# Performance work log

Hardware: AMD Instinct MI355X
Metric: run time of the kernel (lower is better)

The kernel has to match this reference:

```python
import jax, jax.numpy as jnp
import numpy as np

NUM_HEADS = 8
HEAD_DIM = 64  # joiner_dim 512 / 8
LN_EPS = 1e-5


def _layer_norm(x, g, b):
    mu = jnp.mean(x, axis=-1, keepdims=True)
    var = jnp.mean(jnp.square(x - mu), axis=-1, keepdims=True)
    return (x - mu) * jax.lax.rsqrt(var + LN_EPS) * g + b


def setup_inputs() -> dict:
    key = jax.random.key(0)
    ks = jax.random.split(key, 24)
    N, T, S = 16, 512, 5
    E, D, J, V = 512, 512, 512, 2000
    s = 0.02
    inp = {
        "encoder_out": jax.random.normal(ks[0], (N, T, S, E), jnp.float32),
        "decoder_out": jax.random.normal(ks[1], (N, T, S, D), jnp.float32),
        # ScaledLinear projections (initial_scale absorbed into weights)
        "We": jax.random.normal(ks[2], (J, E), jnp.float32) * s * 0.25,
        "be": jnp.zeros((J,), jnp.float32),
        "Wd": jax.random.normal(ks[3], (J, D), jnp.float32) * s * 0.25,
        "bd": jnp.zeros((J,), jnp.float32),
        # LayerNorms
        "g_q": jnp.ones((J,), jnp.float32),
        "beta_q": jnp.zeros((J,), jnp.float32),
        "g_kv": jnp.ones((J,), jnp.float32),
        "beta_kv": jnp.zeros((J,), jnp.float32),
        # attention projections (xavier-ish)
        "Wq": jax.random.normal(ks[4], (J, J), jnp.float32) * s,
        "bq": jnp.zeros((J,), jnp.float32),
        "Wk": jax.random.normal(ks[5], (J, J), jnp.float32) * s,
        "bk": jnp.zeros((J,), jnp.float32),
        "Wv": jax.random.normal(ks[6], (J, J), jnp.float32) * s,
        "bv": jnp.zeros((J,), jnp.float32),
        "Wo": jax.random.normal(ks[7], (J, J), jnp.float32) * s,
        "bo": jnp.zeros((J,), jnp.float32),
        # final vocab projection
        "Wout": jax.random.normal(ks[8], (V, J), jnp.float32) * s,
        "bout": jnp.zeros((V,), jnp.float32),
    }
    return inp


def reference(encoder_out, decoder_out, We, be, Wd, bd, g_q, beta_q, g_kv, beta_kv,
              Wq, bq, Wk, bk, Wv, bv, Wo, bo, Wout, bout):
    # input projections (mode == "transducer", project_input=True)
    enc = jnp.einsum('ntsc,jc->ntsj', encoder_out, We) + be
    dec = jnp.einsum('ntsc,jc->ntsj', decoder_out, Wd) + bd

    # framewise sigmoid attention
    q_in = _layer_norm(dec, g_q, beta_q)
    kv_in = _layer_norm(enc, g_kv, beta_kv)
    q = jnp.einsum('ntsj,kj->ntsk', q_in, Wq) + bq
    k = jnp.einsum('ntsj,kj->ntsk', kv_in, Wk) + bk
    v = jnp.einsum('ntsj,kj->ntsk', kv_in, Wv) + bv

    shp = q.shape[:-1]
    q = q.reshape(*shp, NUM_HEADS, HEAD_DIM)
    k = k.reshape(*shp, NUM_HEADS, HEAD_DIM)
    v = v.reshape(*shp, NUM_HEADS, HEAD_DIM)

    scale = HEAD_DIM ** -0.5
    attn = jax.nn.sigmoid(jnp.sum(q * k, axis=-1, keepdims=True) * scale)  # (N,T,S,H,1)
    context = (attn * v).reshape(*shp, NUM_HEADS * HEAD_DIM)
    context = jnp.einsum('ntsj,kj->ntsk', context, Wo) + bo

    h = jnp.tanh(dec + context)
    logits = jnp.einsum('ntsj,vj->ntsv', h, Wout) + bout
    return logits
```

## Files before the change

kernel.cpp:

```cpp
#include <hip/hip_runtime.h>
#include <stdint.h>


typedef __attribute__((ext_vector_type(8))) __bf16 bf16x8;
typedef __attribute__((ext_vector_type(4))) float float4v;
typedef __attribute__((ext_vector_type(8))) unsigned short ushort8;

static constexpr int M_TOT = 16 * 512 * 5;
static constexpr int JDIM  = 512;
static constexpr int VOUT  = 2000;
static constexpr int VPAD  = 2048;

#define DI __device__ __forceinline__

DI float bf2f(unsigned short u) {
    union { unsigned int i; float f; } w; w.i = ((unsigned int)u) << 16; return w.f;
}
DI unsigned short f2bf(float f) {
    union { float f; unsigned int i; } w; w.f = f;
    return (unsigned short)((w.i + 0x8000u) >> 16);
}

DI void gld_lds16(const void* g, void* l) {
    __builtin_amdgcn_global_load_lds(
        reinterpret_cast<__attribute__((address_space(1))) void*>(
            reinterpret_cast<uintptr_t>(g)),
        reinterpret_cast<__attribute__((address_space(3))) void*>(
            reinterpret_cast<uintptr_t>(l)),
        16, 0, 0);
}

template <int EPI, int NOUT, bool A32>
__global__ __launch_bounds__(256) void gemm_bt(
    const void* __restrict__ Ap, const unsigned short* __restrict__ B,
    const float* __restrict__ bias, void* __restrict__ Cp,
    const unsigned short* __restrict__ dres)
{
    constexpr int K = 512;
    constexpr int BM = 128, BN = 128, BK = 32;
    __shared__ unsigned short As[BM * BK];
    __shared__ unsigned short Bs[BN * BK];

    const int tid  = threadIdx.x;
    const int wave = tid >> 6;
    const int lane = tid & 63;
    const int wm   = wave >> 1;
    const int wn   = wave & 1;
    const int quad = lane >> 4;
    const int l16  = lane & 15;

    const int m0 = blockIdx.y * BM;
    const int n0 = blockIdx.x * BN;

    float4v acc[4][4];
#pragma unroll
    for (int i = 0; i < 4; i++)
#pragma unroll
        for (int j = 0; j < 4; j++)
            acc[i][j] = {0.f, 0.f, 0.f, 0.f};

    const float*          Af = (const float*)Ap;
    const unsigned short* Ab = (const unsigned short*)Ap;

    const int c0 = tid, c1 = tid + 256;
    const int ar0 = c0 >> 2, ac0 = (c0 & 3) * 8;
    const int ar1 = c1 >> 2, ac1 = (c1 & 3) * 8;

    for (int k0 = 0; k0 < K; k0 += BK) {
        gld_lds16(&B[(size_t)(n0 + ar0) * K + k0 + ac0], &Bs[c0 * 8]);
        gld_lds16(&B[(size_t)(n0 + ar1) * K + k0 + ac1], &Bs[c1 * 8]);
        if constexpr (A32) {
            const float* p0 = &Af[(size_t)(m0 + ar0) * K + k0 + ac0];
            const float* p1 = &Af[(size_t)(m0 + ar1) * K + k0 + ac1];
            float4 f0 = *(const float4*)p0;
            float4 f1 = *(const float4*)(p0 + 4);
            float4 g0 = *(const float4*)p1;
            float4 g1 = *(const float4*)(p1 + 4);
            ushort8 u0, u1;
            u0[0] = f2bf(f0.x); u0[1] = f2bf(f0.y); u0[2] = f2bf(f0.z); u0[3] = f2bf(f0.w);
            u0[4] = f2bf(f1.x); u0[5] = f2bf(f1.y); u0[6] = f2bf(f1.z); u0[7] = f2bf(f1.w);
            u1[0] = f2bf(g0.x); u1[1] = f2bf(g0.y); u1[2] = f2bf(g0.z); u1[3] = f2bf(g0.w);
            u1[4] = f2bf(g1.x); u1[5] = f2bf(g1.y); u1[6] = f2bf(g1.z); u1[7] = f2bf(g1.w);
            *reinterpret_cast<ushort8*>(&As[c0 * 8]) = u0;
            *reinterpret_cast<ushort8*>(&As[c1 * 8]) = u1;
        } else {
            gld_lds16(&Ab[(size_t)(m0 + ar0) * K + k0 + ac0], &As[c0 * 8]);
            gld_lds16(&Ab[(size_t)(m0 + ar1) * K + k0 + ac1], &As[c1 * 8]);
        }
        __syncthreads();

        bf16x8 af[4], bfv[4];
#pragma unroll
        for (int i = 0; i < 4; i++)
            af[i] = *reinterpret_cast<const bf16x8*>(
                &As[(wm * 64 + i * 16 + l16) * BK + quad * 8]);
#pragma unroll
        for (int j = 0; j < 4; j++)
            bfv[j] = *reinterpret_cast<const bf16x8*>(
                &Bs[(wn * 64 + j * 16 + l16) * BK + quad * 8]);
#pragma unroll
        for (int i = 0; i < 4; i++)
#pragma unroll
            for (int j = 0; j < 4; j++)
                acc[i][j] = __builtin_amdgcn_mfma_f32_16x16x32_bf16(
                    af[i], bfv[j], acc[i][j], 0, 0, 0);
        __syncthreads();
    }

    float bias_v[4];
#pragma unroll
    for (int j = 0; j < 4; j++) {
        int col = n0 + wn * 64 + j * 16 + l16;
        bias_v[j] = (col < NOUT) ? bias[col] : 0.f;
    }

#pragma unroll
    for (int i = 0; i < 4; i++) {
        int rbase = m0 + wm * 64 + i * 16 + quad * 4;
#pragma unroll
        for (int j = 0; j < 4; j++) {
            int col = n0 + wn * 64 + j * 16 + l16;
#pragma unroll
            for (int r = 0; r < 4; r++) {
                float val = acc[i][j][r] + bias_v[j];
                int row = rbase + r;
                if constexpr (EPI == 0) {
                    ((unsigned short*)Cp)[(size_t)row * NOUT + col] = f2bf(val);
                } else if constexpr (EPI == 2) {
                    float d = bf2f(dres[(size_t)row * 512 + col]);
                    ((unsigned short*)Cp)[(size_t)row * 512 + col] = f2bf(tanhf(d + val));
                } else {
                    if (col < NOUT)
                        ((float*)Cp)[(size_t)row * NOUT + col] = val;
                }
            }
        }
    }
}

__global__ __launch_bounds__(256) void wconv_kernel(
    const float* __restrict__ We, const float* __restrict__ Wd,
    const float* __restrict__ Wq, const float* __restrict__ Wk,
    const float* __restrict__ Wv, const float* __restrict__ Wo,
    const float* __restrict__ Wout, unsigned short* __restrict__ WB)
{
#pragma unroll
    for (int t = 0; t < 4; t++) {
        int i = blockIdx.x * 1024 + t * 256 + threadIdx.x;
        float v;
        if (i < 1572864) {
            int seg = i >> 18, off = i & 262143;
            const float* src = seg == 0 ? We : seg == 1 ? Wd : seg == 2 ? Wq
                             : seg == 3 ? Wk : seg == 4 ? Wv : Wo;
            v = src[off];
        } else {
            int rem = i - 1572864;
            int row = rem >> 9;
            v = (row < VOUT) ? Wout[rem] : 0.f;
        }
        WB[i] = f2bf(v);
    }
}

__global__ __launch_bounds__(256) void ln_kernel(
    const unsigned short* __restrict__ decO, const unsigned short* __restrict__ encO,
    const float* __restrict__ g_q, const float* __restrict__ beta_q,
    const float* __restrict__ g_kv, const float* __restrict__ beta_kv,
    unsigned short* __restrict__ q_in, unsigned short* __restrict__ kv_in)
{
    int row  = blockIdx.x * 4 + (threadIdx.x >> 6);
    int lane = threadIdx.x & 63;
    const unsigned short* src; const float *g, *bt; unsigned short* dst; int r;
    if (row < M_TOT) { src = decO; g = g_q;  bt = beta_q;  dst = q_in;  r = row; }
    else             { src = encO; g = g_kv; bt = beta_kv; dst = kv_in; r = row - M_TOT; }

    ushort8 u = *reinterpret_cast<const ushort8*>(&src[(size_t)r * 512 + lane * 8]);
    float x[8]; float s = 0.f, s2 = 0.f;
#pragma unroll
    for (int j = 0; j < 8; j++) { x[j] = bf2f(u[j]); s += x[j]; s2 += x[j] * x[j]; }
#pragma unroll
    for (int m = 1; m < 64; m <<= 1) {
        s  += __shfl_xor(s, m, 64);
        s2 += __shfl_xor(s2, m, 64);
    }
    float mean = s * (1.f / 512.f);
    float var  = s2 * (1.f / 512.f) - mean * mean;
    float rstd = rsqrtf(var + 1e-5f);
    ushort8 o;
#pragma unroll
    for (int j = 0; j < 8; j++) {
        int col = lane * 8 + j;
        o[j] = f2bf((x[j] - mean) * rstd * g[col] + bt[col]);
    }
    *reinterpret_cast<ushort8*>(&dst[(size_t)r * 512 + lane * 8]) = o;
}

__global__ __launch_bounds__(256) void attn_kernel(
    const unsigned short* __restrict__ q, const unsigned short* __restrict__ k,
    const unsigned short* __restrict__ v, unsigned short* __restrict__ ctx)
{
    int row  = blockIdx.x * 4 + (threadIdx.x >> 6);
    int lane = threadIdx.x & 63;
    size_t off = (size_t)row * 512 + lane * 8;
    ushort8 uq = *reinterpret_cast<const ushort8*>(&q[off]);
    ushort8 uk = *reinterpret_cast<const ushort8*>(&k[off]);
    float dot = 0.f;
#pragma unroll
    for (int j = 0; j < 8; j++) dot += bf2f(uq[j]) * bf2f(uk[j]);
    dot += __shfl_xor(dot, 1, 64);
    dot += __shfl_xor(dot, 2, 64);
    dot += __shfl_xor(dot, 4, 64);
    float sg = 1.f / (1.f + __expf(-dot * 0.125f));
    ushort8 uv = *reinterpret_cast<const ushort8*>(&v[off]);
    ushort8 o;
#pragma unroll
    for (int j = 0; j < 8; j++) o[j] = f2bf(sg * bf2f(uv[j]));
    *reinterpret_cast<ushort8*>(&ctx[off]) = o;
}

extern "C" void kernel_launch(void* const* d_in, const int* in_sizes, int n_in,
                              void* d_out, int out_size, void* d_ws, size_t ws_size,
                              hipStream_t stream)
{
    (void)in_sizes; (void)n_in; (void)out_size; (void)ws_size;
    const float* enc_in  = (const float*)d_in[0];
    const float* dec_in  = (const float*)d_in[1];
    const float* We      = (const float*)d_in[2];  const float* be     = (const float*)d_in[3];
    const float* Wd      = (const float*)d_in[4];  const float* bd     = (const float*)d_in[5];
    const float* g_q     = (const float*)d_in[6];  const float* beta_q = (const float*)d_in[7];
    const float* g_kv    = (const float*)d_in[8];  const float* beta_kv= (const float*)d_in[9];
    const float* Wq      = (const float*)d_in[10]; const float* bq     = (const float*)d_in[11];
    const float* Wk      = (const float*)d_in[12]; const float* bk     = (const float*)d_in[13];
    const float* Wv      = (const float*)d_in[14]; const float* bv     = (const float*)d_in[15];
    const float* Wo      = (const float*)d_in[16]; const float* bo     = (const float*)d_in[17];
    const float* Wout    = (const float*)d_in[18]; const float* bout   = (const float*)d_in[19];
    float* out = (float*)d_out;

    unsigned short* WB    = (unsigned short*)d_ws;
    unsigned short* WeB   = WB + 0;
    unsigned short* WdB   = WB + 262144;
    unsigned short* WqB   = WB + 524288;
    unsigned short* WkB   = WB + 786432;
    unsigned short* WvB   = WB + 1048576;
    unsigned short* WoB   = WB + 1310720;
    unsigned short* WoutB = WB + 1572864;

    char* sbase = (char*)d_ws + 5242880;
    const size_t SZ = (size_t)M_TOT * 512 * 2;
    unsigned short* S0 = (unsigned short*)(sbase + 0 * SZ);
    unsigned short* S1 = (unsigned short*)(sbase + 1 * SZ);
    unsigned short* S2 = (unsigned short*)(sbase + 2 * SZ);
    unsigned short* S3 = (unsigned short*)(sbase + 3 * SZ);
    unsigned short* S4 = (unsigned short*)(sbase + 4 * SZ);
    unsigned short* S5 = (unsigned short*)(sbase + 5 * SZ);

    dim3 blk(256);
    dim3 g512(JDIM / 128, M_TOT / 128);
    dim3 gout(VPAD / 128, M_TOT / 128);

    wconv_kernel<<<2560, blk, 0, stream>>>(We, Wd, Wq, Wk, Wv, Wo, Wout, WB);

    gemm_bt<0, 512, true><<<g512, blk, 0, stream>>>(enc_in, WeB, be, S0, nullptr);
    gemm_bt<0, 512, true><<<g512, blk, 0, stream>>>(dec_in, WdB, bd, S1, nullptr);

    ln_kernel<<<(2 * M_TOT) / 4, blk, 0, stream>>>(S1, S0, g_q, beta_q, g_kv, beta_kv, S2, S3);

    gemm_bt<0, 512, false><<<g512, blk, 0, stream>>>(S2, WqB, bq, S4, nullptr);
    gemm_bt<0, 512, false><<<g512, blk, 0, stream>>>(S3, WkB, bk, S0, nullptr);
    gemm_bt<0, 512, false><<<g512, blk, 0, stream>>>(S3, WvB, bv, S5, nullptr);

    attn_kernel<<<M_TOT / 4, blk, 0, stream>>>(S4, S0, S5, S2);

    gemm_bt<2, 512, false><<<g512, blk, 0, stream>>>(S2, WoB, bo, S3, S1);

    gemm_bt<3, 2000, false><<<gout, blk, 0, stream>>>(S3, WoutB, bout, out, nullptr);
}
```

Baseline: 903.9 us.

## Fold LayerNorm into projection GEMMs, fuse K/V GEMM, swizzle block order

Removes the standalone LayerNorm pass. Row sum and sum-of-squares are accumulated with atomics in the input-projection GEMM epilogue. The normalisation is applied algebraically in the Q and KV GEMM epilogues, using weights pre-scaled by gamma, precomputed row sums of the scaled weights, and biases with beta folded in. K and V are computed by one GEMM with N=1024 and an interleaved output. GEMM blocks are remapped with an XCD-style swizzle. This saves a full read and write of two activations and one launch, at the cost of atomics and slight numerical differences because the mean is subtracted after bf16 rounding.

```diff
diff --git a/kernel.cpp b/kernel.cpp
--- a/kernel.cpp
+++ b/kernel.cpp
@@ -34,7 +34,9 @@
 __global__ __launch_bounds__(256) void gemm_bt(
     const void* __restrict__ Ap, const unsigned short* __restrict__ B,
     const float* __restrict__ bias, void* __restrict__ Cp,
-    const unsigned short* __restrict__ dres)
+    const unsigned short* __restrict__ dres,
+    float* __restrict__ st_sum, float* __restrict__ st_ssq,
+    const float* __restrict__ rs)
 {
     constexpr int K = 512;
     constexpr int BM = 128, BN = 128, BK = 32;
@@ -49,8 +51,12 @@
     const int quad = lane >> 4;
     const int l16  = lane & 15;
 
-    const int m0 = blockIdx.y * BM;
-    const int n0 = blockIdx.x * BN;
+    const int gx      = gridDim.x;
+    const int nwg     = gx * gridDim.y;
+    const int id      = blockIdx.x + gx * blockIdx.y;
+    const int logical = (id & 7) * (nwg >> 3) + (id >> 3);
+    const int m0 = (logical / gx) * BM;
+    const int n0 = (logical % gx) * BN;
 
     float4v acc[4][4];
 #pragma unroll
@@ -107,31 +113,82 @@
         __syncthreads();
     }
 
-    float bias_v[4];
+    float bias_v[4], rs_v[4];
 #pragma unroll
     for (int j = 0; j < 4; j++) {
         int col = n0 + wn * 64 + j * 16 + l16;
         bias_v[j] = (col < NOUT) ? bias[col] : 0.f;
-    }
-
-#pragma unroll
-    for (int i = 0; i < 4; i++) {
-        int rbase = m0 + wm * 64 + i * 16 + quad * 4;
-#pragma unroll
-        for (int j = 0; j < 4; j++) {
-            int col = n0 + wn * 64 + j * 16 + l16;
+        if constexpr (EPI == 4) rs_v[j] = rs[col];
+    }
+
+    if constexpr (EPI == 4) {
+#pragma unroll
+        for (int i = 0; i < 4; i++) {
+            int rbase = m0 + wm * 64 + i * 16 + quad * 4;
 #pragma unroll
             for (int r = 0; r < 4; r++) {
-                float val = acc[i][j][r] + bias_v[j];
                 int row = rbase + r;
-                if constexpr (EPI == 0) {
+                float s  = st_sum[row];
+                float s2 = st_ssq[row];
+                float mean = s * (1.f / 512.f);
+                float var  = s2 * (1.f / 512.f) - mean * mean;
+                float rstd = rsqrtf(var + 1e-5f);
+                float crow = -mean * rstd;
+#pragma unroll
+                for (int j = 0; j < 4; j++) {
+                    int col = n0 + wn * 64 + j * 16 + l16;
+                    float val = fmaf(rstd, acc[i][j][r],
+                                fmaf(crow, rs_v[j], bias_v[j]));
                     ((unsigned short*)Cp)[(size_t)row * NOUT + col] = f2bf(val);
-                } else if constexpr (EPI == 2) {
-                    float d = bf2f(dres[(size_t)row * 512 + col]);
-                    ((unsigned short*)Cp)[(size_t)row * 512 + col] = f2bf(tanhf(d + val));
-                } else {
-                    if (col < NOUT)
-                        ((float*)Cp)[(size_t)row * NOUT + col] = val;
+                }
+            }
+        }
+    } else {
+#pragma unroll
+        for (int i = 0; i < 4; i++) {
+            int rbase = m0 + wm * 64 + i * 16 + quad * 4;
+#pragma unroll
+            for (int j = 0; j < 4; j++) {
+                int col = n0 + wn * 64 + j * 16 + l16;
+#pragma unroll
+                for (int r = 0; r < 4; r++) {
+                    float val = acc[i][j][r] + bias_v[j];
+                    int row = rbase + r;
+                    if constexpr (EPI == 2) {
+                        float d = bf2f(dres[(size_t)row * 512 + col]);
+                        ((unsigned short*)Cp)[(size_t)row * 512 + col] = f2bf(tanhf(d + val));
+                    } else if constexpr (EPI == 3) {
+                        if (col < NOUT)
+                            ((float*)Cp)[(size_t)row * NOUT + col] = val;
+                    } else {
+                        ((unsigned short*)Cp)[(size_t)row * NOUT + col] = f2bf(val);
+                    }
+                }
+            }
+        }
+    }
+
+    if constexpr (EPI == 6) {
+#pragma unroll
+        for (int i = 0; i < 4; i++) {
+#pragma unroll
+            for (int r = 0; r < 4; r++) {
+                float ps = 0.f, ps2 = 0.f;
+#pragma unroll
+                for (int j = 0; j < 4; j++) {
+                    float v = acc[i][j][r] + bias_v[j];
+                    ps += v;
+                    ps2 = fmaf(v, v, ps2);
+                }
+#pragma unroll
+                for (int m = 1; m < 16; m <<= 1) {
+                    ps  += __shfl_xor(ps,  m, 64);
+                    ps2 += __shfl_xor(ps2, m, 64);
+                }
+                if (l16 == 0) {
+                    int row = m0 + wm * 64 + i * 16 + quad * 4 + r;
+                    atomicAdd(&st_sum[row], ps);
+                    atomicAdd(&st_ssq[row], ps2);
                 }
             }
         }
@@ -142,7 +199,9 @@
     const float* __restrict__ We, const float* __restrict__ Wd,
     const float* __restrict__ Wq, const float* __restrict__ Wk,
     const float* __restrict__ Wv, const float* __restrict__ Wo,
-    const float* __restrict__ Wout, unsigned short* __restrict__ WB)
+    const float* __restrict__ Wout,
+    const float* __restrict__ g_q, const float* __restrict__ g_kv,
+    unsigned short* __restrict__ WB, float* __restrict__ stz)
 {
 #pragma unroll
     for (int t = 0; t < 4; t++) {
@@ -153,6 +212,9 @@
             const float* src = seg == 0 ? We : seg == 1 ? Wd : seg == 2 ? Wq
                              : seg == 3 ? Wk : seg == 4 ? Wv : Wo;
             v = src[off];
+            int j = off & 511;
+            if (seg == 2)                 v *= g_q[j];
+            else if (seg == 3 || seg == 4) v *= g_kv[j];
         } else {
             int rem = i - 1572864;
             int row = rem >> 9;
@@ -160,50 +222,61 @@
         }
         WB[i] = f2bf(v);
     }
-}
-
-__global__ __launch_bounds__(256) void ln_kernel(
-    const unsigned short* __restrict__ decO, const unsigned short* __restrict__ encO,
+    int z = blockIdx.x * 256 + threadIdx.x;
+    if (z < 163840) stz[z] = 0.f;
+}
+
+__global__ __launch_bounds__(256) void lnprep_kernel(
+    const float* __restrict__ Wq, const float* __restrict__ Wk,
+    const float* __restrict__ Wv,
     const float* __restrict__ g_q, const float* __restrict__ beta_q,
     const float* __restrict__ g_kv, const float* __restrict__ beta_kv,
-    unsigned short* __restrict__ q_in, unsigned short* __restrict__ kv_in)
+    const float* __restrict__ bq, const float* __restrict__ bk,
+    const float* __restrict__ bv,
+    float* __restrict__ rs_q, float* __restrict__ b_q,
+    float* __restrict__ rs_kv, float* __restrict__ b_kv)
+{
+    int idx  = blockIdx.x * 4 + (threadIdx.x >> 6);
+    int lane = threadIdx.x & 63;
+    const float *W, *g, *bt, *bb; float *rs_out, *b_out; int r;
+    if (idx < 512)       { W = Wq; g = g_q;  bt = beta_q;  bb = bq;
+                           rs_out = &rs_q[idx];        b_out = &b_q[idx];        r = idx; }
+    else if (idx < 1024) { W = Wk; g = g_kv; bt = beta_kv; bb = bk;
+                           rs_out = &rs_kv[idx - 512]; b_out = &b_kv[idx - 512]; r = idx - 512; }
+    else                 { W = Wv; g = g_kv; bt = beta_kv; bb = bv;
+                           rs_out = &rs_kv[idx - 512]; b_out = &b_kv[idx - 512]; r = idx - 1024; }
+
+    const float* wr = &W[(size_t)r * 512];
+    float s = 0.f, sb = 0.f;
+    int j0 = lane * 8;
+    float4 w0 = *(const float4*)&wr[j0];
+    float4 w1 = *(const float4*)&wr[j0 + 4];
+    float4 ga = *(const float4*)&g[j0];
+    float4 gb = *(const float4*)&g[j0 + 4];
+    float4 ba = *(const float4*)&bt[j0];
+    float4 bb4 = *(const float4*)&bt[j0 + 4];
+    s  += w0.x * ga.x + w0.y * ga.y + w0.z * ga.z + w0.w * ga.w;
+    s  += w1.x * gb.x + w1.y * gb.y + w1.z * gb.z + w1.w * gb.w;
+    sb += w0.x * ba.x + w0.y * ba.y + w0.z * ba.z + w0.w * ba.w;
+    sb += w1.x * bb4.x + w1.y * bb4.y + w1.z * bb4.z + w1.w * bb4.w;
+#pragma unroll
+    for (int m = 1; m < 64; m <<= 1) {
+        s  += __shfl_xor(s,  m, 64);
+        sb += __shfl_xor(sb, m, 64);
+    }
+    if (lane == 0) { *rs_out = s; *b_out = bb[r] + sb; }
+}
+
+__global__ __launch_bounds__(256) void attn_kernel(
+    const unsigned short* __restrict__ q, const unsigned short* __restrict__ kv,
+    unsigned short* __restrict__ ctx)
 {
     int row  = blockIdx.x * 4 + (threadIdx.x >> 6);
     int lane = threadIdx.x & 63;
-    const unsigned short* src; const float *g, *bt; unsigned short* dst; int r;
-    if (row < M_TOT) { src = decO; g = g_q;  bt = beta_q;  dst = q_in;  r = row; }
-    else             { src = encO; g = g_kv; bt = beta_kv; dst = kv_in; r = row - M_TOT; }
-
-    ushort8 u = *reinterpret_cast<const ushort8*>(&src[(size_t)r * 512 + lane * 8]);
-    float x[8]; float s = 0.f, s2 = 0.f;
-#pragma unroll
-    for (int j = 0; j < 8; j++) { x[j] = bf2f(u[j]); s += x[j]; s2 += x[j] * x[j]; }
-#pragma unroll
-    for (int m = 1; m < 64; m <<= 1) {
-        s  += __shfl_xor(s, m, 64);
-        s2 += __shfl_xor(s2, m, 64);
-    }
-    float mean = s * (1.f / 512.f);
-    float var  = s2 * (1.f / 512.f) - mean * mean;
-    float rstd = rsqrtf(var + 1e-5f);
-    ushort8 o;
-#pragma unroll
-    for (int j = 0; j < 8; j++) {
-        int col = lane * 8 + j;
-        o[j] = f2bf((x[j] - mean) * rstd * g[col] + bt[col]);
-    }
-    *reinterpret_cast<ushort8*>(&dst[(size_t)r * 512 + lane * 8]) = o;
-}
-
-__global__ __launch_bounds__(256) void attn_kernel(
-    const unsigned short* __restrict__ q, const unsigned short* __restrict__ k,
-    const unsigned short* __restrict__ v, unsigned short* __restrict__ ctx)
-{
-    int row  = blockIdx.x * 4 + (threadIdx.x >> 6);
-    int lane = threadIdx.x & 63;
-    size_t off = (size_t)row * 512 + lane * 8;
-    ushort8 uq = *reinterpret_cast<const ushort8*>(&q[off]);
-    ushort8 uk = *reinterpret_cast<const ushort8*>(&k[off]);
+    size_t qoff = (size_t)row * 512 + lane * 8;
+    size_t kvo  = (size_t)row * 1024 + lane * 8;
+    ushort8 uq = *reinterpret_cast<const ushort8*>(&q[qoff]);
+    ushort8 uk = *reinterpret_cast<const ushort8*>(&kv[kvo]);
     float dot = 0.f;
 #pragma unroll
     for (int j = 0; j < 8; j++) dot += bf2f(uq[j]) * bf2f(uk[j]);
@@ -211,11 +284,11 @@
     dot += __shfl_xor(dot, 2, 64);
     dot += __shfl_xor(dot, 4, 64);
     float sg = 1.f / (1.f + __expf(-dot * 0.125f));
-    ushort8 uv = *reinterpret_cast<const ushort8*>(&v[off]);
+    ushort8 uv = *reinterpret_cast<const ushort8*>(&kv[kvo + 512]);
     ushort8 o;
 #pragma unroll
     for (int j = 0; j < 8; j++) o[j] = f2bf(sg * bf2f(uv[j]));
-    *reinterpret_cast<ushort8*>(&ctx[off]) = o;
+    *reinterpret_cast<ushort8*>(&ctx[qoff]) = o;
 }
 
 extern "C" void kernel_launch(void* const* d_in, const int* in_sizes, int n_in,
@@ -241,7 +314,6 @@
     unsigned short* WdB   = WB + 262144;
     unsigned short* WqB   = WB + 524288;
     unsigned short* WkB   = WB + 786432;
-    unsigned short* WvB   = WB + 1048576;
     unsigned short* WoB   = WB + 1310720;
     unsigned short* WoutB = WB + 1572864;
 
@@ -254,24 +326,41 @@
     unsigned short* S4 = (unsigned short*)(sbase + 4 * SZ);
     unsigned short* S5 = (unsigned short*)(sbase + 5 * SZ);
 
+    float* stf  = (float*)(sbase + 5 * SZ);
+    float* sumD = stf;
+    float* ssqD = stf + 40960;
+    float* sumE = stf + 81920;
+    float* ssqE = stf + 122880;
+    float* rs_q  = stf + 163840;
+    float* b_q   = stf + 164352;
+    float* rs_kv = stf + 164864;
+    float* b_kv  = stf + 165888;
+
     dim3 blk(256);
     dim3 g512(JDIM / 128, M_TOT / 128);
+    dim3 g1024(1024 / 128, M_TOT / 128);
     dim3 gout(VPAD / 128, M_TOT / 128);
 
-    wconv_kernel<<<2560, blk, 0, stream>>>(We, Wd, Wq, Wk, Wv, Wo, Wout, WB);
-
-    gemm_bt<0, 512, true><<<g512, blk, 0, stream>>>(enc_in, WeB, be, S0, nullptr);
-    gemm_bt<0, 512, true><<<g512, blk, 0, stream>>>(dec_in, WdB, bd, S1, nullptr);
-
-    ln_kernel<<<(2 * M_TOT) / 4, blk, 0, stream>>>(S1, S0, g_q, beta_q, g_kv, beta_kv, S2, S3);
-
-    gemm_bt<0, 512, false><<<g512, blk, 0, stream>>>(S2, WqB, bq, S4, nullptr);
-    gemm_bt<0, 512, false><<<g512, blk, 0, stream>>>(S3, WkB, bk, S0, nullptr);
-    gemm_bt<0, 512, false><<<g512, blk, 0, stream>>>(S3, WvB, bv, S5, nullptr);
-
-    attn_kernel<<<M_TOT / 4, blk, 0, stream>>>(S4, S0, S5, S2);
-
-    gemm_bt<2, 512, false><<<g512, blk, 0, stream>>>(S2, WoB, bo, S3, S1);
-
-    gemm_bt<3, 2000, false><<<gout, blk, 0, stream>>>(S3, WoutB, bout, out, nullptr);
-}
+    wconv_kernel<<<2560, blk, 0, stream>>>(We, Wd, Wq, Wk, Wv, Wo, Wout,
+                                           g_q, g_kv, WB, stf);
+    lnprep_kernel<<<384, blk, 0, stream>>>(Wq, Wk, Wv, g_q, beta_q, g_kv, beta_kv,
+                                           bq, bk, bv, rs_q, b_q, rs_kv, b_kv);
+
+    gemm_bt<6, 512, true><<<g512, blk, 0, stream>>>(enc_in, WeB, be, S0, nullptr,
+                                                    sumE, ssqE, nullptr);
+    gemm_bt<6, 512, true><<<g512, blk, 0, stream>>>(dec_in, WdB, bd, S1, nullptr,
+                                                    sumD, ssqD, nullptr);
+
+    gemm_bt<4, 512, false><<<g512, blk, 0, stream>>>(S1, WqB, b_q, S4, nullptr,
+                                                     sumD, ssqD, rs_q);
+    gemm_bt<4, 1024, false><<<g1024, blk, 0, stream>>>(S0, WkB, b_kv, S2, nullptr,
+                                                       sumE, ssqE, rs_kv);
+
+    attn_kernel<<<M_TOT / 4, blk, 0, stream>>>(S4, S2, S5);
+
+    gemm_bt<2, 512, false><<<g512, blk, 0, stream>>>(S5, WoB, bo, S3, S1,
+                                                     nullptr, nullptr, nullptr);
+
+    gemm_bt<3, 2000, false><<<gout, blk, 0, stream>>>(S3, WoutB, bout, out, nullptr,
+                                                      nullptr, nullptr, nullptr);
+}
```

Result: no change. 888.5 us (-1.7%).
